# Optimization experiments

Hardware: AMD Instinct MI355X
Metric: run time of the kernel (lower is better)

## Reference

```python
import jax, jax.numpy as jnp
import numpy as np

B = 128          # batch (stands in for bit-packed words)
C, H, W = 3, 32, 32
K = 64           # num_kernels
RFS, STRIDE = 5, 1
HO = (H - RFS) // STRIDE + 1   # 28
P = HO * HO                     # 784 output positions
G0 = 8                          # 2**tree_depth, tree_depth=3
NL1, NL2, NCLS = 64000, 32000, 10

# ALL_OPERATIONS order; each gate is multilinear: c0 + ca*a + cb*b + cab*a*b
COEF = jnp.array([
    [0, 0, 0, 0],    # zero
    [0, 0, 0, 1],    # and
    [0, 1, 0, -1],   # not_implies (a & ~b)
    [0, 1, 0, 0],    # a
    [0, 0, 1, -1],   # not_implied_by (b & ~a)
    [0, 0, 1, 0],    # b
    [0, 1, 1, -2],   # xor
    [0, 1, 1, -1],   # or
    [1, -1, -1, 1],  # not_or
    [1, -1, -1, 2],  # not_xor
    [1, 0, -1, 0],   # not_b
    [1, 0, -1, 1],   # implied_by (~b | a)
    [1, -1, 0, 0],   # not_a
    [1, -1, 0, 1],   # implies (~a | b)
    [1, 0, 0, -1],   # not_and
    [1, 0, 0, 0],    # one
], dtype=jnp.float32)


def _gate(a, b, ops):
    # ops: int array broadcastable against a/b trailing dims
    c = COEF[ops]  # [..., 4]
    return c[..., 0] + c[..., 1] * a + c[..., 2] * b + c[..., 3] * (a * b)


def _forward(x, cl, cr, o0, o1, o2, o3, a1, b1, p1, a2, b2, p2):
    # Conv logic layer: gather level-0 operand pairs -> [B, K, P, G0]
    la = jnp.take(x, cl, axis=1)
    lb = jnp.take(x, cr, axis=1)
    g = _gate(la, lb, o0[:, None, :])            # ops per (kernel, gate)
    # Binary tree reduction: level l pairs gates (2i, 2i+1)
    for ops in (o1, o2, o3):
        g = _gate(g[..., 0::2], g[..., 1::2], ops[:, None, :])
    z = g[..., 0].reshape(x.shape[0], K * P)     # [B, 50176]
    # Logic linear layers: out[i] = gate(in[a[i]], in[b[i]], op[i])
    z = _gate(z[:, a1], z[:, b1], p1)            # [B, NL1]
    z = _gate(z[:, a2], z[:, b2], p2)            # [B, NL2]
    # GroupSum: popcount per class group
    return z.reshape(z.shape[0], NCLS, -1).sum(-1)  # [B, 10]


def setup_inputs() -> dict:
    key = jax.random.key(0)
    x = (jax.random.uniform(key, (B, C * H * W)) < 0.5).astype(jnp.float32)
    rng = np.random.default_rng(0)
    bh = np.repeat(np.arange(HO), HO)  # h_pos per position
    bw = np.tile(np.arange(HO), HO)    # w_pos per position

    def conv_idx():
        dh = rng.integers(0, RFS, (K, P, G0))
        dw = rng.integers(0, RFS, (K, P, G0))
        dc = rng.integers(0, C, (K, P, G0))
        idx = dc * H * W + (bh[None, :, None] * STRIDE + dh) * W + (bw[None, :, None] * STRIDE + dw)
        return jnp.asarray(idx.astype(np.int32))

    ops = lambda shape: jnp.asarray(rng.integers(0, 16, shape).astype(np.int32))
    ridx = lambda hi, n: jnp.asarray(rng.integers(0, hi, n).astype(np.int32))
    return {
        'x': x,
        'conv_left_idx': conv_idx(), 'conv_right_idx': conv_idx(),
        'conv_ops0': ops((K, G0)), 'conv_ops1': ops((K, 4)),
        'conv_ops2': ops((K, 2)), 'conv_ops3': ops((K, 1)),
        'lin1_a': ridx(K * P, NL1), 'lin1_b': ridx(K * P, NL1), 'lin1_ops': ops((NL1,)),
        'lin2_a': ridx(NL1, NL2), 'lin2_b': ridx(NL1, NL2), 'lin2_ops': ops((NL2,)),
    }


def reference(x, conv_left_idx, conv_right_idx, conv_ops0, conv_ops1, conv_ops2, conv_ops3,
              lin1_a, lin1_b, lin1_ops, lin2_a, lin2_b, lin2_ops):
    return _forward(x, conv_left_idx, conv_right_idx, conv_ops0, conv_ops1, conv_ops2, conv_ops3,
                    lin1_a, lin1_b, lin1_ops, lin2_a, lin2_b, lin2_ops)
```

## Files before the change

### kernel.cpp

```cpp
#include <hip/hip_runtime.h>
#include <stdint.h>

#define NFEAT 3072
#define NWORD 2
#define NK 64
#define NP 784
#define NG 8
#define KP (NK * NP)
#define NL1 64000
#define NL2 32000
#define NCLS 10
#define NB 128
#define JBLK 128

__device__ __forceinline__ uint64_t bsel(uint64_t x, uint64_t p, uint64_t q) {
    return (x & p) | (~x & q);
}
__device__ __forceinline__ ulonglong2 gate128(ulonglong2 A, ulonglong2 B, int op) {
    uint64_t m3 = (uint64_t)0 - (uint64_t)((op >> 0) & 1);
    uint64_t m2 = (uint64_t)0 - (uint64_t)((op >> 1) & 1);
    uint64_t m1 = (uint64_t)0 - (uint64_t)((op >> 2) & 1);
    uint64_t m0 = (uint64_t)0 - (uint64_t)((op >> 3) & 1);
    ulonglong2 r;
    r.x = bsel(A.x, bsel(B.x, m3, m2), bsel(B.x, m1, m0));
    r.y = bsel(A.y, bsel(B.y, m3, m2), bsel(B.y, m1, m0));
    return r;
}

__global__ __launch_bounds__(256) void pack_kernel(const float* __restrict__ x,
                                                   uint64_t* __restrict__ xb,
                                                   float* __restrict__ out) {
    int t = blockIdx.x * blockDim.x + threadIdx.x;
    if (t < NB * NCLS) out[t] = 0.0f;
    if (t >= NFEAT * NWORD) return;
    int f = t % NFEAT;
    int w = t / NFEAT;
    uint64_t v = 0;
#pragma unroll 8
    for (int j = 0; j < 64; ++j) {
        float val = x[(size_t)(w * 64 + j) * NFEAT + f];
        v |= (uint64_t)(val != 0.0f) << j;
    }
    xb[f * NWORD + w] = v;
}

__global__ __launch_bounds__(256) void conv_kernel(
    const uint64_t* __restrict__ xb,
    const int* __restrict__ cl, const int* __restrict__ cr,
    const int* __restrict__ o0, const int* __restrict__ o1,
    const int* __restrict__ o2, const int* __restrict__ o3,
    uint64_t* __restrict__ z) {
    __shared__ uint64_t sxb[NFEAT * NWORD];
    {
        ulonglong2* s2 = reinterpret_cast<ulonglong2*>(sxb);
        const ulonglong2* g2 = reinterpret_cast<const ulonglong2*>(xb);
        for (int i = threadIdx.x; i < NFEAT; i += blockDim.x)
            s2[i] = g2[i];
    }
    __syncthreads();

    int t = blockIdx.x * blockDim.x + threadIdx.x;
    if (t >= KP) return;
    int k = t / NP;

    const int4* cl4 = reinterpret_cast<const int4*>(cl + (size_t)t * NG);
    const int4* cr4 = reinterpret_cast<const int4*>(cr + (size_t)t * NG);
    int4 l0 = cl4[0], l1 = cl4[1];
    int4 r0 = cr4[0], r1 = cr4[1];
    int la[NG] = {l0.x, l0.y, l0.z, l0.w, l1.x, l1.y, l1.z, l1.w};
    int rb[NG] = {r0.x, r0.y, r0.z, r0.w, r1.x, r1.y, r1.z, r1.w};

    int op0[NG], op1[4], op2[2], op3;
#pragma unroll
    for (int g = 0; g < NG; ++g) op0[g] = o0[k * NG + g];
#pragma unroll
    for (int g = 0; g < 4; ++g) op1[g] = o1[k * 4 + g];
#pragma unroll
    for (int g = 0; g < 2; ++g) op2[g] = o2[k * 2 + g];
    op3 = o3[k];

    const ulonglong2* sxb2 = reinterpret_cast<const ulonglong2*>(sxb);
    ulonglong2 gg[NG];
#pragma unroll
    for (int g = 0; g < NG; ++g) {
        ulonglong2 va = sxb2[la[g]];
        ulonglong2 vb = sxb2[rb[g]];
        gg[g] = gate128(va, vb, op0[g]);
    }
#pragma unroll
    for (int g = 0; g < 4; ++g)
        gg[g] = gate128(gg[2 * g], gg[2 * g + 1], op1[g]);
#pragma unroll
    for (int g = 0; g < 2; ++g)
        gg[g] = gate128(gg[2 * g], gg[2 * g + 1], op2[g]);
    reinterpret_cast<ulonglong2*>(z)[t] = gate128(gg[0], gg[1], op3);
}

__global__ __launch_bounds__(JBLK) void lin2_fused_kernel(
    const uint64_t* __restrict__ z,
    const int* __restrict__ a1, const int* __restrict__ b1,
    const int* __restrict__ p1,
    const int* __restrict__ a2, const int* __restrict__ b2,
    const int* __restrict__ p2, float* __restrict__ out) {
    __shared__ alignas(16) uint64_t s[NWORD][JBLK];
    int blk = blockIdx.x;
    const int chunks_per_cls = (NL2 / NCLS) / JBLK;
    int c = blk / chunks_per_cls;
    int j = c * (NL2 / NCLS) + (blk % chunks_per_cls) * JBLK + threadIdx.x;

    int ia = a2[j], ib = b2[j], op = p2[j];
    int iaa = a1[ia], iab = b1[ia], opa = p1[ia];
    int iba = a1[ib], ibb = b1[ib], opb = p1[ib];
    const ulonglong2* z2p = reinterpret_cast<const ulonglong2*>(z);
    ulonglong2 za = gate128(z2p[iaa], z2p[iab], opa);
    ulonglong2 zb = gate128(z2p[iba], z2p[ibb], opb);
    ulonglong2 zz = gate128(za, zb, op);
    s[0][threadIdx.x] = zz.x;
    s[1][threadIdx.x] = zz.y;
    __syncthreads();

    int bb = threadIdx.x;
    int w = bb >> 6, sh = bb & 63;
    const ulonglong2* sp = reinterpret_cast<const ulonglong2*>(s[w]);
    int cnt = 0;
#pragma unroll 16
    for (int jj = 0; jj < JBLK / 2; ++jj) {
        ulonglong2 v = sp[jj];
        cnt += (int)((v.x >> sh) & 1) + (int)((v.y >> sh) & 1);
    }
    atomicAdd(&out[bb * NCLS + c], (float)cnt);
}

extern "C" void kernel_launch(void* const* d_in, const int* in_sizes, int n_in,
                              void* d_out, int out_size, void* d_ws, size_t ws_size,
                              hipStream_t stream) {
    const float* x  = (const float*)d_in[0];
    const int* cl   = (const int*)d_in[1];
    const int* cr   = (const int*)d_in[2];
    const int* o0   = (const int*)d_in[3];
    const int* o1   = (const int*)d_in[4];
    const int* o2   = (const int*)d_in[5];
    const int* o3   = (const int*)d_in[6];
    const int* a1   = (const int*)d_in[7];
    const int* b1   = (const int*)d_in[8];
    const int* p1   = (const int*)d_in[9];
    const int* a2   = (const int*)d_in[10];
    const int* b2   = (const int*)d_in[11];
    const int* p2   = (const int*)d_in[12];
    float* out = (float*)d_out;

    uint8_t* ws = (uint8_t*)d_ws;
    uint64_t* xb = (uint64_t*)(ws);
    uint64_t* z  = (uint64_t*)(ws + 64 * 1024);

    pack_kernel<<<(NFEAT * NWORD + 255) / 256, 256, 0, stream>>>(x, xb, out);
    conv_kernel<<<(KP + 255) / 256, 256, 0, stream>>>(xb, cl, cr, o0, o1, o2, o3, z);
    lin2_fused_kernel<<<NL2 / JBLK, JBLK, 0, stream>>>(z, a1, b1, p1, a2, b2, p2, out);
}
```

Measured before the change: 99.04 us.

## Split 128-bit word work across thread pairs and pack bits with wave ballot

Each conv and lin2 work item is now handled by two threads, one per 64-bit word, instead of one thread doing both words. This doubles thread-level parallelism and latency hiding for the gather-heavy kernels, at the cost of loading indices and ops twice. The pack kernel now uses one thread per sample bit and a wavefront ballot (64-wide on this hardware) in place of a serial 64-iteration loop. The popcount phase in lin2 is split across two thread halves that each process half the block's entries and then atomically add their partial counts.

```diff
diff --git a/kernel.cpp b/kernel.cpp
--- a/kernel.cpp
+++ b/kernel.cpp
@@ -13,35 +13,28 @@
 #define NB 128
 #define JBLK 128
 
-__device__ __forceinline__ uint64_t bsel(uint64_t x, uint64_t p, uint64_t q) {
+__device__ __forceinline__ uint64_t bsel64(uint64_t x, uint64_t p, uint64_t q) {
     return (x & p) | (~x & q);
 }
-__device__ __forceinline__ ulonglong2 gate128(ulonglong2 A, ulonglong2 B, int op) {
+__device__ __forceinline__ uint64_t gate64(uint64_t A, uint64_t B, int op) {
     uint64_t m3 = (uint64_t)0 - (uint64_t)((op >> 0) & 1);
     uint64_t m2 = (uint64_t)0 - (uint64_t)((op >> 1) & 1);
     uint64_t m1 = (uint64_t)0 - (uint64_t)((op >> 2) & 1);
     uint64_t m0 = (uint64_t)0 - (uint64_t)((op >> 3) & 1);
-    ulonglong2 r;
-    r.x = bsel(A.x, bsel(B.x, m3, m2), bsel(B.x, m1, m0));
-    r.y = bsel(A.y, bsel(B.y, m3, m2), bsel(B.y, m1, m0));
-    return r;
+    return bsel64(A, bsel64(B, m3, m2), bsel64(B, m1, m0));
 }
 
 __global__ __launch_bounds__(256) void pack_kernel(const float* __restrict__ x,
                                                    uint64_t* __restrict__ xb,
                                                    float* __restrict__ out) {
-    int t = blockIdx.x * blockDim.x + threadIdx.x;
-    if (t < NB * NCLS) out[t] = 0.0f;
-    if (t >= NFEAT * NWORD) return;
-    int f = t % NFEAT;
-    int w = t / NFEAT;
-    uint64_t v = 0;
-#pragma unroll 8
-    for (int j = 0; j < 64; ++j) {
-        float val = x[(size_t)(w * 64 + j) * NFEAT + f];
-        v |= (uint64_t)(val != 0.0f) << j;
-    }
-    xb[f * NWORD + w] = v;
+    int gt = blockIdx.x * 256 + threadIdx.x;
+    if (gt < NB * NCLS) out[gt] = 0.0f;
+    int fw = gt >> 6;
+    int lane = gt & 63;
+    int f = fw >> 1, w = fw & 1;
+    float val = x[(size_t)(w * 64 + lane) * NFEAT + f];
+    uint64_t m = __ballot(val != 0.0f);
+    if (lane == 0) xb[f * NWORD + w] = m;
 }
 
 __global__ __launch_bounds__(256) void conv_kernel(
@@ -59,12 +52,13 @@
     }
     __syncthreads();
 
-    int t = blockIdx.x * blockDim.x + threadIdx.x;
-    if (t >= KP) return;
-    int k = t / NP;
+    int tid = blockIdx.x * 256 + threadIdx.x;
+    int item = tid >> 1;
+    int w = tid & 1;
+    int k = item / NP;
 
-    const int4* cl4 = reinterpret_cast<const int4*>(cl + (size_t)t * NG);
-    const int4* cr4 = reinterpret_cast<const int4*>(cr + (size_t)t * NG);
+    const int4* cl4 = reinterpret_cast<const int4*>(cl + (size_t)item * NG);
+    const int4* cr4 = reinterpret_cast<const int4*>(cr + (size_t)item * NG);
     int4 l0 = cl4[0], l1 = cl4[1];
     int4 r0 = cr4[0], r1 = cr4[1];
     int la[NG] = {l0.x, l0.y, l0.z, l0.w, l1.x, l1.y, l1.z, l1.w};
@@ -79,24 +73,20 @@
     for (int g = 0; g < 2; ++g) op2[g] = o2[k * 2 + g];
     op3 = o3[k];
 
-    const ulonglong2* sxb2 = reinterpret_cast<const ulonglong2*>(sxb);
-    ulonglong2 gg[NG];
+    uint64_t gg[NG];
 #pragma unroll
-    for (int g = 0; g < NG; ++g) {
-        ulonglong2 va = sxb2[la[g]];
-        ulonglong2 vb = sxb2[rb[g]];
-        gg[g] = gate128(va, vb, op0[g]);
-    }
+    for (int g = 0; g < NG; ++g)
+        gg[g] = gate64(sxb[la[g] * NWORD + w], sxb[rb[g] * NWORD + w], op0[g]);
 #pragma unroll
     for (int g = 0; g < 4; ++g)
-        gg[g] = gate128(gg[2 * g], gg[2 * g + 1], op1[g]);
+        gg[g] = gate64(gg[2 * g], gg[2 * g + 1], op1[g]);
 #pragma unroll
     for (int g = 0; g < 2; ++g)
-        gg[g] = gate128(gg[2 * g], gg[2 * g + 1], op2[g]);
-    reinterpret_cast<ulonglong2*>(z)[t] = gate128(gg[0], gg[1], op3);
+        gg[g] = gate64(gg[2 * g], gg[2 * g + 1], op2[g]);
+    z[(size_t)item * NWORD + w] = gate64(gg[0], gg[1], op3);
 }
 
-__global__ __launch_bounds__(JBLK) void lin2_fused_kernel(
+__global__ __launch_bounds__(256) void lin2_fused_kernel(
     const uint64_t* __restrict__ z,
     const int* __restrict__ a1, const int* __restrict__ b1,
     const int* __restrict__ p1,
@@ -106,25 +96,24 @@
     int blk = blockIdx.x;
     const int chunks_per_cls = (NL2 / NCLS) / JBLK;
     int c = blk / chunks_per_cls;
-    int j = c * (NL2 / NCLS) + (blk % chunks_per_cls) * JBLK + threadIdx.x;
+
+    int jloc = threadIdx.x >> 1;
+    int w = threadIdx.x & 1;
+    int j = c * (NL2 / NCLS) + (blk % chunks_per_cls) * JBLK + jloc;
 
     int ia = a2[j], ib = b2[j], op = p2[j];
-    int iaa = a1[ia], iab = b1[ia], opa = p1[ia];
-    int iba = a1[ib], ibb = b1[ib], opb = p1[ib];
-    const ulonglong2* z2p = reinterpret_cast<const ulonglong2*>(z);
-    ulonglong2 za = gate128(z2p[iaa], z2p[iab], opa);
-    ulonglong2 zb = gate128(z2p[iba], z2p[ibb], opb);
-    ulonglong2 zz = gate128(za, zb, op);
-    s[0][threadIdx.x] = zz.x;
-    s[1][threadIdx.x] = zz.y;
+    uint64_t za = gate64(z[(size_t)a1[ia] * NWORD + w], z[(size_t)b1[ia] * NWORD + w], p1[ia]);
+    uint64_t zb = gate64(z[(size_t)a1[ib] * NWORD + w], z[(size_t)b1[ib] * NWORD + w], p1[ib]);
+    s[w][jloc] = gate64(za, zb, op);
     __syncthreads();
 
-    int bb = threadIdx.x;
-    int w = bb >> 6, sh = bb & 63;
-    const ulonglong2* sp = reinterpret_cast<const ulonglong2*>(s[w]);
+    int bb = threadIdx.x & 127;
+    int half = threadIdx.x >> 7;
+    int wq = bb >> 6, sh = bb & 63;
+    const ulonglong2* sp = reinterpret_cast<const ulonglong2*>(s[wq]) + half * (JBLK / 4);
     int cnt = 0;
-#pragma unroll 16
-    for (int jj = 0; jj < JBLK / 2; ++jj) {
+#pragma unroll
+    for (int jj = 0; jj < JBLK / 4; ++jj) {
         ulonglong2 v = sp[jj];
         cnt += (int)((v.x >> sh) & 1) + (int)((v.y >> sh) & 1);
     }
@@ -153,7 +142,7 @@
     uint64_t* xb = (uint64_t*)(ws);
     uint64_t* z  = (uint64_t*)(ws + 64 * 1024);
 
-    pack_kernel<<<(NFEAT * NWORD + 255) / 256, 256, 0, stream>>>(x, xb, out);
-    conv_kernel<<<(KP + 255) / 256, 256, 0, stream>>>(xb, cl, cr, o0, o1, o2, o3, z);
-    lin2_fused_kernel<<<NL2 / JBLK, JBLK, 0, stream>>>(z, a1, b1, p1, a2, b2, p2, out);
+    pack_kernel<<<(NFEAT * NWORD * 64) / 256, 256, 0, stream>>>(x, xb, out);
+    conv_kernel<<<(KP * NWORD) / 256, 256, 0, stream>>>(xb, cl, cr, o0, o1, o2, o3, z);
+    lin2_fused_kernel<<<NL2 / JBLK, 256, 0, stream>>>(z, a1, b1, p1, a2, b2, p2, out);
 }
```

Result: slower. 104.6 us (+5.7%).
